# Kernel optimization log

Hardware: AMD Instinct MI355X
Metric: run time of the kernel (lower is better)

Reference implementation:

```python
import jax, jax.numpy as jnp
import numpy as np

EMBED = 1024
HEADS = 16
HEAD_DIM = EMBED // HEADS


def setup_inputs() -> dict:
    key = jax.random.key(0)
    ks = jax.random.split(key, 6)
    N, S = 4, 1024
    query = jax.random.normal(ks[0], (N, S, EMBED), dtype=jnp.float32)
    keys = jax.random.normal(ks[1], (N, S, EMBED), dtype=jnp.float32)
    values = jax.random.normal(ks[2], (N, S, EMBED), dtype=jnp.float32)
    mask = jax.random.randint(ks[3], (N, 1, S, S), 0, 2, dtype=jnp.int32)
    W_out = jax.random.normal(ks[4], (EMBED, EMBED), dtype=jnp.float32) * (1.0 / np.sqrt(EMBED))
    b_out = jax.random.normal(ks[5], (EMBED,), dtype=jnp.float32) * 0.02
    return {"query": query, "keys": keys, "values": values, "mask": mask,
            "W_out": W_out, "b_out": b_out}


def reference(query, keys, values, mask, W_out, b_out):
    N, Q, _ = query.shape
    K = keys.shape[1]
    # NOTE: the torch module never applies its per-head q/k/v Linear layers;
    # only the reshape + attention + fc_out are in the forward path.
    q = query.reshape(N, Q, HEADS, HEAD_DIM)
    k = keys.reshape(N, K, HEADS, HEAD_DIM)
    v = values.reshape(N, K, HEADS, HEAD_DIM)
    # energy: [N, H, Q, K]
    energy = jnp.einsum("bqhd,bkhd->bhqk", q, k)
    energy = jnp.where(mask == 0, jnp.float32(-1e20), energy)
    attn = jax.nn.softmax(energy / jnp.sqrt(jnp.float32(HEAD_DIM)), axis=3)
    out = jnp.einsum("bhqk,bkhd->bqhd", attn, v).reshape(N, Q, HEADS * HEAD_DIM)
    return out @ W_out.T + b_out
```

## Files before the change

kernel.cpp:

```cpp
#include <hip/hip_runtime.h>
#include <math.h>

#define NB 4
#define SL 1024
#define EMB 1024
#define NH 16
#define HD 64
#define QB 128

typedef __attribute__((ext_vector_type(8))) short bf16x8;
typedef __attribute__((ext_vector_type(4))) float f32x4;

static __device__ __forceinline__ unsigned pk2(float a, float b) {
    unsigned x = __float_as_uint(a) + 0x8000u;
    unsigned y = __float_as_uint(b) + 0x8000u;
    return (x >> 16) | (y & 0xFFFF0000u);
}
static __device__ __forceinline__ float exp2_fast(float x) {
    float r; asm("v_exp_f32 %0, %1" : "=v"(r) : "v"(x)); return r;
}
static __device__ __forceinline__ void gload_lds16(const void* g, void* l) {
    __builtin_amdgcn_global_load_lds(
        (const __attribute__((address_space(1))) unsigned int*)g,
        (__attribute__((address_space(3))) unsigned int*)l, 16, 0, 0);
}

__global__ __launch_bounds__(256) void prep(
    const float* __restrict__ W, unsigned short* __restrict__ Wb,
    const float* __restrict__ Kf, unsigned short* __restrict__ Kb,
    const float* __restrict__ V, unsigned short* __restrict__ Vt,
    const int* __restrict__ mask, unsigned long long* __restrict__ Mbt)
{
    __shared__ unsigned short sT[128 * 68];
    const int bid = blockIdx.x, tid = threadIdx.x;

    if (bid < 512) {
        int i = (bid * 256 + tid) * 8;
        float4 f0 = *(const float4*)&W[i];
        float4 f1 = *(const float4*)&W[i + 4];
        uint4 u = { pk2(f0.x,f0.y), pk2(f0.z,f0.w), pk2(f1.x,f1.y), pk2(f1.z,f1.w) };
        *(uint4*)&Wb[i] = u;
    } else if (bid < 2560) {
        int t = bid - 512;
        int b = t >> 9, h = (t >> 5) & 15, k0 = (t & 31) * 32;
        int r = tid >> 3, d = (tid & 7) * 8;
        const float* gp = &Kf[((size_t)(b * SL + k0 + r)) * EMB + h * HD + d];
        float4 f0 = *(const float4*)gp, f1 = *(const float4*)(gp + 4);
        uint4 u = { pk2(f0.x,f0.y), pk2(f0.z,f0.w), pk2(f1.x,f1.y), pk2(f1.z,f1.w) };
        *(uint4*)&Kb[((size_t)((b * NH + h) * SL + k0 + r)) * HD + d] = u;
    } else if (bid < 3072) {
        int t = bid - 2560;
        int bh = t >> 3, kb = t & 7;
        int b = bh >> 4, h = bh & 15;
        int k0 = kb * 128;
        #pragma unroll
        for (int i = 0; i < 4; ++i) {
            int lin = (i * 256 + tid) * 8;
            int r = lin >> 6, d = lin & 63;
            const float* gp = &V[((size_t)(b * SL + k0 + r)) * EMB + h * HD + d];
            float4 f0 = *(const float4*)gp, f1 = *(const float4*)(gp + 4);
            uint2 u0 = { pk2(f0.x,f0.y), pk2(f0.z,f0.w) };
            uint2 u1 = { pk2(f1.x,f1.y), pk2(f1.z,f1.w) };
            *(uint2*)&sT[r * 68 + d]     = u0;
            *(uint2*)&sT[r * 68 + d + 4] = u1;
        }
        __syncthreads();
        #pragma unroll
        for (int p = 0; p < 4; ++p) {
            int d = p * 16 + (tid >> 4);
            int c = tid & 15;
            unsigned v[4];
            #pragma unroll
            for (int j = 0; j < 4; ++j) {
                unsigned lo = sT[(c * 8 + 2 * j) * 68 + d];
                unsigned hi = sT[(c * 8 + 2 * j + 1) * 68 + d];
                v[j] = lo | (hi << 16);
            }
            uint4 u = { v[0], v[1], v[2], v[3] };
            *(uint4*)&Vt[((size_t)(bh * HD + d)) * SL + k0 + c * 8] = u;
        }
    } else {
        int t = bid - 3072;
        int lane = tid & 63;
        #pragma unroll
        for (int r = 0; r < 4; ++r) {
            int wid = (t * 4 + (tid >> 6)) * 4 + r;
            int c = wid & 15, q = (wid >> 4) & 1023, bb = wid >> 14;
            int mv = mask[((size_t)bb * SL + q) * SL + c * 64 + lane];
            unsigned long long bits = __ballot(mv != 0);
            if (lane == 0) Mbt[((size_t)bb * 16 + c) * SL + q] = bits;
        }
    }
}

__global__ __launch_bounds__(256, 2) void attn_mfma(
    const float* __restrict__ Q, const unsigned short* __restrict__ Kb,
    const unsigned short* __restrict__ Vt,
    const unsigned long long* __restrict__ Mbt,
    unsigned short* __restrict__ Oa)
{
    const int q0 = blockIdx.x * QB;
    const int h = blockIdx.y, b = blockIdx.z;
    const int tid = threadIdx.x;
    const int w = tid >> 6, lane = tid & 63;
    const int m16 = lane & 15, quad = lane >> 4;
    const int lr = lane >> 3, lc = lane & 7;
    const int sr0 = tid >> 3;

    __shared__ __align__(16) unsigned short sQ[QB * 64];
    __shared__ __align__(16) unsigned short sK[2][64 * 64];
    __shared__ __align__(16) unsigned short sVt[2][64 * 64];
    __shared__ __align__(16) unsigned short sP[QB * 72];
    __shared__ uint2 lut[16];

    if (tid < 16) {
        unsigned w0 = ((tid & 1) ? 0xFFFFu : 0u) | ((tid & 2) ? 0xFFFF0000u : 0u);
        unsigned w1 = ((tid & 4) ? 0xFFFFu : 0u) | ((tid & 8) ? 0xFFFF0000u : 0u);
        lut[tid] = make_uint2(w0, w1);
    }

    const size_t vbase = (size_t)((b * NH + h) * HD) * SL;
    const size_t kbase = (size_t)((b * NH + h) * SL) * HD;

    #pragma unroll
    for (int i = 0; i < 2; ++i) {
        int row = w * 16 + i * 8;
        gload_lds16(&Vt[vbase + (size_t)(row + lr) * SL + (lc ^ lr) * 8], &sVt[0][row * 64]);
        gload_lds16(&Kb[kbase + (size_t)(row + lr) * HD + (lc ^ lr) * 8], &sK[0][row * 64]);
    }
    #pragma unroll
    for (int it = 0; it < 4; ++it) {
        int r = sr0 + it * 32;
        const float* gp = &Q[((size_t)(b * SL + q0 + r)) * EMB + h * HD + lc * 8];
        float4 f0 = *(const float4*)gp, f1 = *(const float4*)(gp + 4);
        uint4 u = { pk2(f0.x,f0.y), pk2(f0.z,f0.w), pk2(f1.x,f1.y), pk2(f1.z,f1.w) };
        *(uint4*)&sQ[r * 64 + ((lc ^ (r & 7)) * 8)] = u;
    }
    __syncthreads();

    bf16x8 bQ[2][2];
    #pragma unroll
    for (int u = 0; u < 2; ++u) {
        int qrow = w * 32 + u * 16 + m16;
        #pragma unroll
        for (int hh = 0; hh < 2; ++hh)
            bQ[u][hh] = *(const bf16x8*)&sQ[qrow * 64 + (((hh * 4 + quad) ^ (qrow & 7)) * 8)];
    }

    f32x4 O[2][4] = {};
    f32x4 lacc[2] = {};
    const float CSC = 0.125f * 1.44269504f;
    const short one_bf = (short)0x3F80;
    const bf16x8 ones = { one_bf, one_bf, one_bf, one_bf, one_bf, one_bf, one_bf, one_bf };

    for (int kt = 0; kt < 16; ++kt) {
        const int bf = kt & 1;
        if (kt < 15) {
            const int k0n = (kt + 1) * 64;
            #pragma unroll
            for (int i = 0; i < 2; ++i) {
                int row = w * 16 + i * 8;
                gload_lds16(&Vt[vbase + (size_t)(row + lr) * SL + k0n + (lc ^ lr) * 8],
                            &sVt[bf ^ 1][row * 64]);
                gload_lds16(&Kb[kbase + (size_t)(k0n + row + lr) * HD + (lc ^ lr) * 8],
                            &sK[bf ^ 1][row * 64]);
            }
        }
        unsigned long long mb0 = Mbt[(size_t)(b * 16 + kt) * SL + q0 + w * 32 + m16];
        unsigned long long mb1 = Mbt[(size_t)(b * 16 + kt) * SL + q0 + w * 32 + 16 + m16];

        f32x4 sc[2][4];
        #pragma unroll
        for (int t = 0; t < 4; ++t) {
            int krow = t * 16 + m16;
            bf16x8 a0 = *(const bf16x8*)&sK[bf][krow * 64 + ((quad ^ (krow & 7)) * 8)];
            bf16x8 a1 = *(const bf16x8*)&sK[bf][krow * 64 + (((4 + quad) ^ (krow & 7)) * 8)];
            f32x4 z = {0.f, 0.f, 0.f, 0.f};
            sc[0][t] = __builtin_amdgcn_mfma_f32_16x16x32_bf16(a0, bQ[0][0], z,        0,0,0);
            sc[0][t] = __builtin_amdgcn_mfma_f32_16x16x32_bf16(a1, bQ[0][1], sc[0][t], 0,0,0);
            sc[1][t] = __builtin_amdgcn_mfma_f32_16x16x32_bf16(a0, bQ[1][0], z,        0,0,0);
            sc[1][t] = __builtin_amdgcn_mfma_f32_16x16x32_bf16(a1, bQ[1][1], sc[1][t], 0,0,0);
        }

        #pragma unroll
        for (int u = 0; u < 2; ++u) {
            unsigned long long mb = u ? mb1 : mb0;
            unsigned wlo = (unsigned)mb, whi = (unsigned)(mb >> 32);
            unsigned short* pr = &sP[(w * 32 + u * 16 + m16) * 72];
            #pragma unroll
            for (int t = 0; t < 4; ++t) {
                unsigned word = (t < 2) ? wlo : whi;
                unsigned nib = (word >> ((t & 1) * 16 + quad * 4)) & 0xFu;
                uint2 am = lut[nib];
                uint2 pw;
                pw.x = pk2(exp2_fast(sc[u][t][0] * CSC), exp2_fast(sc[u][t][1] * CSC)) & am.x;
                pw.y = pk2(exp2_fast(sc[u][t][2] * CSC), exp2_fast(sc[u][t][3] * CSC)) & am.y;
                *(uint2*)&pr[t * 16 + quad * 4] = pw;
            }
        }
        asm volatile("s_waitcnt lgkmcnt(0)" ::: "memory");

        bf16x8 bP[2][2];
        #pragma unroll
        for (int u = 0; u < 2; ++u)
            #pragma unroll
            for (int hh = 0; hh < 2; ++hh)
                bP[u][hh] = *(const bf16x8*)&sP[(w * 32 + u * 16 + m16) * 72 + hh * 32 + quad * 8];

        lacc[0] = __builtin_amdgcn_mfma_f32_16x16x32_bf16(ones, bP[0][0], lacc[0], 0,0,0);
        lacc[0] = __builtin_amdgcn_mfma_f32_16x16x32_bf16(ones, bP[0][1], lacc[0], 0,0,0);
        lacc[1] = __builtin_amdgcn_mfma_f32_16x16x32_bf16(ones, bP[1][0], lacc[1], 0,0,0);
        lacc[1] = __builtin_amdgcn_mfma_f32_16x16x32_bf16(ones, bP[1][1], lacc[1], 0,0,0);

        #pragma unroll
        for (int dt = 0; dt < 4; ++dt) {
            int drow = dt * 16 + m16;
            bf16x8 v0 = *(const bf16x8*)&sVt[bf][drow * 64 + ((quad ^ (drow & 7)) * 8)];
            bf16x8 v1 = *(const bf16x8*)&sVt[bf][drow * 64 + (((4 + quad) ^ (drow & 7)) * 8)];
            O[0][dt] = __builtin_amdgcn_mfma_f32_16x16x32_bf16(v0, bP[0][0], O[0][dt], 0,0,0);
            O[0][dt] = __builtin_amdgcn_mfma_f32_16x16x32_bf16(v1, bP[0][1], O[0][dt], 0,0,0);
            O[1][dt] = __builtin_amdgcn_mfma_f32_16x16x32_bf16(v0, bP[1][0], O[1][dt], 0,0,0);
            O[1][dt] = __builtin_amdgcn_mfma_f32_16x16x32_bf16(v1, bP[1][1], O[1][dt], 0,0,0);
        }

        __syncthreads();
    }

    #pragma unroll
    for (int u = 0; u < 2; ++u) {
        float inv = 1.f / lacc[u][0];
        size_t base = ((size_t)(b * SL + q0 + w * 32 + u * 16 + m16)) * EMB + h * HD + quad * 4;
        #pragma unroll
        for (int dt = 0; dt < 4; ++dt) {
            uint2 ow = { pk2(O[u][dt][0] * inv, O[u][dt][1] * inv),
                         pk2(O[u][dt][2] * inv, O[u][dt][3] * inv) };
            *(uint2*)&Oa[base + dt * 16] = ow;
        }
    }
}

__global__ __launch_bounds__(512, 2) void proj_mfma(
    const unsigned short* __restrict__ A, const unsigned short* __restrict__ Wb,
    const float* __restrict__ bias, float* __restrict__ C)
{
    const int n0 = blockIdx.x * 128;
    const int m0 = blockIdx.y * 128;
    const int tid = threadIdx.x;
    const int w = tid >> 6, lane = tid & 63;
    const int m16 = lane & 15, quad = lane >> 4;
    const int lr = lane >> 3, lc = lane & 7;
    const int wm = (w >> 2) * 64, wn = (w & 3) * 32;

    __shared__ __align__(16) unsigned short sA[2][128 * 64];
    __shared__ __align__(16) unsigned short sW[2][128 * 64];

    f32x4 acc[4][2] = {};

    #pragma unroll
    for (int i = 0; i < 2; ++i) {
        int r = w * 16 + i * 8;
        gload_lds16(&A [(size_t)(m0 + r + lr) * EMB + (lc ^ lr) * 8], &sA[0][r * 64]);
        gload_lds16(&Wb[(size_t)(n0 + r + lr) * EMB + (lc ^ lr) * 8], &sW[0][r * 64]);
    }
    __syncthreads();

    for (int it = 0; it < 16; ++it) {
        const int bf = it & 1;
        if (it < 15) {
            int e0 = (it + 1) * 64;
            #pragma unroll
            for (int i = 0; i < 2; ++i) {
                int r = w * 16 + i * 8;
                gload_lds16(&A [(size_t)(m0 + r + lr) * EMB + e0 + (lc ^ lr) * 8], &sA[bf ^ 1][r * 64]);
                gload_lds16(&Wb[(size_t)(n0 + r + lr) * EMB + e0 + (lc ^ lr) * 8], &sW[bf ^ 1][r * 64]);
            }
        }
        #pragma unroll
        for (int hh = 0; hh < 2; ++hh) {
            bf16x8 af[4], bw[2];
            #pragma unroll
            for (int mt = 0; mt < 4; ++mt) {
                int r = wm + mt * 16 + m16;
                af[mt] = *(const bf16x8*)&sA[bf][r * 64 + (((hh * 4 + quad) ^ (r & 7)) * 8)];
            }
            #pragma unroll
            for (int nt = 0; nt < 2; ++nt) {
                int r = wn + nt * 16 + m16;
                bw[nt] = *(const bf16x8*)&sW[bf][r * 64 + (((hh * 4 + quad) ^ (r & 7)) * 8)];
            }
            #pragma unroll
            for (int mt = 0; mt < 4; ++mt)
                #pragma unroll
                for (int nt = 0; nt < 2; ++nt)
                    acc[mt][nt] = __builtin_amdgcn_mfma_f32_16x16x32_bf16(af[mt], bw[nt], acc[mt][nt], 0,0,0);
        }
        __syncthreads();
    }

    #pragma unroll
    for (int nt = 0; nt < 2; ++nt) {
        float bv = bias[n0 + wn + nt * 16 + m16];
        #pragma unroll
        for (int mt = 0; mt < 4; ++mt) {
            size_t row = (size_t)(m0 + wm + mt * 16 + quad * 4);
            #pragma unroll
            for (int rg = 0; rg < 4; ++rg)
                C[(row + rg) * EMB + n0 + wn + nt * 16 + m16] = acc[mt][nt][rg] + bv;
        }
    }
}

extern "C" void kernel_launch(void* const* d_in, const int* in_sizes, int n_in,
                              void* d_out, int out_size, void* d_ws, size_t ws_size,
                              hipStream_t stream) {
    const float* Q    = (const float*)d_in[0];
    const float* K    = (const float*)d_in[1];
    const float* V    = (const float*)d_in[2];
    const int*   mask = (const int*)  d_in[3];
    const float* W    = (const float*)d_in[4];
    const float* bias = (const float*)d_in[5];

    unsigned short* Oa = (unsigned short*)d_ws;
    unsigned short* Wb = Oa + (size_t)NB * SL * EMB;
    unsigned long long* Mbt = (unsigned long long*)(Wb + (size_t)EMB * EMB);
    unsigned short* Vt = (unsigned short*)(Mbt + (size_t)NB * 16 * SL);
    unsigned short* Kb = Vt + (size_t)NB * NH * HD * SL;

    prep<<<7168, 256, 0, stream>>>(W, Wb, K, Kb, V, Vt, mask, Mbt);
    attn_mfma<<<dim3(SL / QB, NH, NB), 256, 0, stream>>>(Q, Kb, Vt, Mbt, Oa);
    proj_mfma<<<dim3(EMB / 128, (NB * SL) / 128), 512, 0, stream>>>(Oa, Wb, bias, (float*)d_out);
}
```

Baseline: 166.0 us.

## Pre-convert Q to bf16 in prep, share Q/P LDS buffer, remap attention blocks

Q is now converted to bf16 in a head-major layout inside the prep kernel, so the attention kernel loads it with direct global-to-LDS copies instead of fp32 loads plus in-kernel packing. The Q and P shared-memory buffers are merged into one, which needs an extra barrier after Q is read into registers. The mask LUT is replaced by bitwise computation, and the grid is flattened with a block remap that groups 8 heads per query tile, likely for L2 reuse. The trade is extra prep traffic for writing and re-reading Qb, against less LDS per block, which may allow higher occupancy.

Result: slower. 172.4 us (+3.9%).

```diff
diff --git a/kernel.cpp b/kernel.cpp
--- a/kernel.cpp
+++ b/kernel.cpp
@@ -28,6 +28,7 @@
 __global__ __launch_bounds__(256) void prep(
     const float* __restrict__ W, unsigned short* __restrict__ Wb,
     const float* __restrict__ Kf, unsigned short* __restrict__ Kb,
+    const float* __restrict__ Qf, unsigned short* __restrict__ Qb,
     const float* __restrict__ V, unsigned short* __restrict__ Vt,
     const int* __restrict__ mask, unsigned long long* __restrict__ Mbt)
 {
@@ -40,16 +41,19 @@
         float4 f1 = *(const float4*)&W[i + 4];
         uint4 u = { pk2(f0.x,f0.y), pk2(f0.z,f0.w), pk2(f1.x,f1.y), pk2(f1.z,f1.w) };
         *(uint4*)&Wb[i] = u;
-    } else if (bid < 2560) {
+    } else if (bid < 4608) {
         int t = bid - 512;
+        const float* src = Kf;
+        unsigned short* dst = Kb;
+        if (t >= 2048) { t -= 2048; src = Qf; dst = Qb; }
         int b = t >> 9, h = (t >> 5) & 15, k0 = (t & 31) * 32;
         int r = tid >> 3, d = (tid & 7) * 8;
-        const float* gp = &Kf[((size_t)(b * SL + k0 + r)) * EMB + h * HD + d];
+        const float* gp = &src[((size_t)(b * SL + k0 + r)) * EMB + h * HD + d];
         float4 f0 = *(const float4*)gp, f1 = *(const float4*)(gp + 4);
         uint4 u = { pk2(f0.x,f0.y), pk2(f0.z,f0.w), pk2(f1.x,f1.y), pk2(f1.z,f1.w) };
-        *(uint4*)&Kb[((size_t)((b * NH + h) * SL + k0 + r)) * HD + d] = u;
-    } else if (bid < 3072) {
-        int t = bid - 2560;
+        *(uint4*)&dst[((size_t)((b * NH + h) * SL + k0 + r)) * HD + d] = u;
+    } else if (bid < 5120) {
+        int t = bid - 4608;
         int bh = t >> 3, kb = t & 7;
         int b = bh >> 4, h = bh & 15;
         int k0 = kb * 128;
@@ -80,7 +84,7 @@
             *(uint4*)&Vt[((size_t)(bh * HD + d)) * SL + k0 + c * 8] = u;
         }
     } else {
-        int t = bid - 3072;
+        int t = bid - 5120;
         int lane = tid & 63;
         #pragma unroll
         for (int r = 0; r < 4; ++r) {
@@ -94,30 +98,24 @@
 }
 
 __global__ __launch_bounds__(256, 2) void attn_mfma(
-    const float* __restrict__ Q, const unsigned short* __restrict__ Kb,
+    const unsigned short* __restrict__ Qb, const unsigned short* __restrict__ Kb,
     const unsigned short* __restrict__ Vt,
     const unsigned long long* __restrict__ Mbt,
     unsigned short* __restrict__ Oa)
 {
-    const int q0 = blockIdx.x * QB;
-    const int h = blockIdx.y, b = blockIdx.z;
+    const int bid = blockIdx.x;
+    const int bh  = ((bid >> 6) << 3) | (bid & 7);
+    const int q0  = ((bid >> 3) & 7) * QB;
+    const int b = bh >> 4, h = bh & 15;
+
     const int tid = threadIdx.x;
     const int w = tid >> 6, lane = tid & 63;
     const int m16 = lane & 15, quad = lane >> 4;
     const int lr = lane >> 3, lc = lane & 7;
-    const int sr0 = tid >> 3;
-
-    __shared__ __align__(16) unsigned short sQ[QB * 64];
+
+    __shared__ __align__(16) unsigned short sQP[QB * 72];
     __shared__ __align__(16) unsigned short sK[2][64 * 64];
     __shared__ __align__(16) unsigned short sVt[2][64 * 64];
-    __shared__ __align__(16) unsigned short sP[QB * 72];
-    __shared__ uint2 lut[16];
-
-    if (tid < 16) {
-        unsigned w0 = ((tid & 1) ? 0xFFFFu : 0u) | ((tid & 2) ? 0xFFFF0000u : 0u);
-        unsigned w1 = ((tid & 4) ? 0xFFFFu : 0u) | ((tid & 8) ? 0xFFFF0000u : 0u);
-        lut[tid] = make_uint2(w0, w1);
-    }
 
     const size_t vbase = (size_t)((b * NH + h) * HD) * SL;
     const size_t kbase = (size_t)((b * NH + h) * SL) * HD;
@@ -129,12 +127,9 @@
         gload_lds16(&Kb[kbase + (size_t)(row + lr) * HD + (lc ^ lr) * 8], &sK[0][row * 64]);
     }
     #pragma unroll
-    for (int it = 0; it < 4; ++it) {
-        int r = sr0 + it * 32;
-        const float* gp = &Q[((size_t)(b * SL + q0 + r)) * EMB + h * HD + lc * 8];
-        float4 f0 = *(const float4*)gp, f1 = *(const float4*)(gp + 4);
-        uint4 u = { pk2(f0.x,f0.y), pk2(f0.z,f0.w), pk2(f1.x,f1.y), pk2(f1.z,f1.w) };
-        *(uint4*)&sQ[r * 64 + ((lc ^ (r & 7)) * 8)] = u;
+    for (int i = 0; i < 4; ++i) {
+        int row = w * 32 + i * 8;
+        gload_lds16(&Qb[kbase + (size_t)(q0 + row + lr) * HD + (lc ^ lr) * 8], &sQP[row * 64]);
     }
     __syncthreads();
 
@@ -144,8 +139,9 @@
         int qrow = w * 32 + u * 16 + m16;
         #pragma unroll
         for (int hh = 0; hh < 2; ++hh)
-            bQ[u][hh] = *(const bf16x8*)&sQ[qrow * 64 + (((hh * 4 + quad) ^ (qrow & 7)) * 8)];
-    }
+            bQ[u][hh] = *(const bf16x8*)&sQP[qrow * 64 + (((hh * 4 + quad) ^ (qrow & 7)) * 8)];
+    }
+    __syncthreads();
 
     f32x4 O[2][4] = {};
     f32x4 lacc[2] = {};
@@ -186,15 +182,16 @@
         for (int u = 0; u < 2; ++u) {
             unsigned long long mb = u ? mb1 : mb0;
             unsigned wlo = (unsigned)mb, whi = (unsigned)(mb >> 32);
-            unsigned short* pr = &sP[(w * 32 + u * 16 + m16) * 72];
+            unsigned short* pr = &sQP[(w * 32 + u * 16 + m16) * 72];
             #pragma unroll
             for (int t = 0; t < 4; ++t) {
                 unsigned word = (t < 2) ? wlo : whi;
                 unsigned nib = (word >> ((t & 1) * 16 + quad * 4)) & 0xFu;
-                uint2 am = lut[nib];
+                unsigned am0 = ((nib & 1u) ? 0xFFFFu : 0u) | ((nib & 2u) ? 0xFFFF0000u : 0u);
+                unsigned am1 = ((nib & 4u) ? 0xFFFFu : 0u) | ((nib & 8u) ? 0xFFFF0000u : 0u);
                 uint2 pw;
-                pw.x = pk2(exp2_fast(sc[u][t][0] * CSC), exp2_fast(sc[u][t][1] * CSC)) & am.x;
-                pw.y = pk2(exp2_fast(sc[u][t][2] * CSC), exp2_fast(sc[u][t][3] * CSC)) & am.y;
+                pw.x = pk2(exp2_fast(sc[u][t][0] * CSC), exp2_fast(sc[u][t][1] * CSC)) & am0;
+                pw.y = pk2(exp2_fast(sc[u][t][2] * CSC), exp2_fast(sc[u][t][3] * CSC)) & am1;
                 *(uint2*)&pr[t * 16 + quad * 4] = pw;
             }
         }
@@ -205,7 +202,7 @@
         for (int u = 0; u < 2; ++u)
             #pragma unroll
             for (int hh = 0; hh < 2; ++hh)
-                bP[u][hh] = *(const bf16x8*)&sP[(w * 32 + u * 16 + m16) * 72 + hh * 32 + quad * 8];
+                bP[u][hh] = *(const bf16x8*)&sQP[(w * 32 + u * 16 + m16) * 72 + hh * 32 + quad * 8];
 
         lacc[0] = __builtin_amdgcn_mfma_f32_16x16x32_bf16(ones, bP[0][0], lacc[0], 0,0,0);
         lacc[0] = __builtin_amdgcn_mfma_f32_16x16x32_bf16(ones, bP[0][1], lacc[0], 0,0,0);
@@ -325,8 +322,9 @@
     unsigned long long* Mbt = (unsigned long long*)(Wb + (size_t)EMB * EMB);
     unsigned short* Vt = (unsigned short*)(Mbt + (size_t)NB * 16 * SL);
     unsigned short* Kb = Vt + (size_t)NB * NH * HD * SL;
-
-    prep<<<7168, 256, 0, stream>>>(W, Wb, K, Kb, V, Vt, mask, Mbt);
-    attn_mfma<<<dim3(SL / QB, NH, NB), 256, 0, stream>>>(Q, Kb, Vt, Mbt, Oa);
+    unsigned short* Qbuf = Kb + (size_t)NB * NH * SL * HD;
+
+    prep<<<9216, 256, 0, stream>>>(W, Wb, K, Kb, Q, Qbuf, V, Vt, mask, Mbt);
+    attn_mfma<<<512, 256, 0, stream>>>(Qbuf, Kb, Vt, Mbt, Oa);
     proj_mfma<<<dim3(EMB / 128, (NB * SL) / 128), 512, 0, stream>>>(Oa, Wb, bias, (float*)d_out);
 }
```

## Halve attention query tile, reuse Q LDS for P, raise occupancy and swizzle grid

Applied to the files above, without the earlier changes.

Shrinks the attention query block from 128 to 64 rows so each wave handles 16 query rows, doubling the block count to 1024 and raising launch bounds to 4 blocks per CU. The sQ buffer is reused as the P staging buffer, and the mask LUT in LDS is replaced by inline bit computation, which cuts LDS footprint. A 1D grid with a remapped block index groups blocks so those sharing K/V run close together. This aims at better latency hiding and L2 reuse, at the cost of reloading K/V tiles for twice as many blocks and fewer MFMAs per K/V load.

New measurement: 167.5 us. Within noise of the previous version (+0.9%).

```diff
diff --git a/kernel.cpp b/kernel.cpp
--- a/kernel.cpp
+++ b/kernel.cpp
@@ -6,7 +6,7 @@
 #define EMB 1024
 #define NH 16
 #define HD 64
-#define QB 128
+#define QB 64
 
 typedef __attribute__((ext_vector_type(8))) short bf16x8;
 typedef __attribute__((ext_vector_type(4))) float f32x4;
@@ -93,31 +93,26 @@
     }
 }
 
-__global__ __launch_bounds__(256, 2) void attn_mfma(
-    const float* __restrict__ Q, const unsigned short* __restrict__ Kb,
+__global__ __launch_bounds__(256, 4) void attn_mfma(
+    const float* __restrict__ Qf, const unsigned short* __restrict__ Kb,
     const unsigned short* __restrict__ Vt,
     const unsigned long long* __restrict__ Mbt,
     unsigned short* __restrict__ Oa)
 {
-    const int q0 = blockIdx.x * QB;
-    const int h = blockIdx.y, b = blockIdx.z;
+    const int bid = blockIdx.x;
+    const int bh  = ((bid >> 7) << 3) | (bid & 7);
+    const int q0  = ((bid >> 3) & 15) * QB;
+    const int b = bh >> 4, h = bh & 15;
+
     const int tid = threadIdx.x;
     const int w = tid >> 6, lane = tid & 63;
     const int m16 = lane & 15, quad = lane >> 4;
     const int lr = lane >> 3, lc = lane & 7;
     const int sr0 = tid >> 3;
 
-    __shared__ __align__(16) unsigned short sQ[QB * 64];
-    __shared__ __align__(16) unsigned short sK[2][64 * 64];
+    __shared__ __align__(16) unsigned short sQP[QB * 64];
+    __shared__ __align__(16) unsigned short sK [2][64 * 64];
     __shared__ __align__(16) unsigned short sVt[2][64 * 64];
-    __shared__ __align__(16) unsigned short sP[QB * 72];
-    __shared__ uint2 lut[16];
-
-    if (tid < 16) {
-        unsigned w0 = ((tid & 1) ? 0xFFFFu : 0u) | ((tid & 2) ? 0xFFFF0000u : 0u);
-        unsigned w1 = ((tid & 4) ? 0xFFFFu : 0u) | ((tid & 8) ? 0xFFFF0000u : 0u);
-        lut[tid] = make_uint2(w0, w1);
-    }
 
     const size_t vbase = (size_t)((b * NH + h) * HD) * SL;
     const size_t kbase = (size_t)((b * NH + h) * SL) * HD;
@@ -129,26 +124,24 @@
         gload_lds16(&Kb[kbase + (size_t)(row + lr) * HD + (lc ^ lr) * 8], &sK[0][row * 64]);
     }
     #pragma unroll
-    for (int it = 0; it < 4; ++it) {
+    for (int it = 0; it < 2; ++it) {
         int r = sr0 + it * 32;
-        const float* gp = &Q[((size_t)(b * SL + q0 + r)) * EMB + h * HD + lc * 8];
+        const float* gp = &Qf[((size_t)(b * SL + q0 + r)) * EMB + h * HD + lc * 8];
         float4 f0 = *(const float4*)gp, f1 = *(const float4*)(gp + 4);
         uint4 u = { pk2(f0.x,f0.y), pk2(f0.z,f0.w), pk2(f1.x,f1.y), pk2(f1.z,f1.w) };
-        *(uint4*)&sQ[r * 64 + ((lc ^ (r & 7)) * 8)] = u;
+        *(uint4*)&sQP[r * 64 + ((lc ^ (r & 7)) * 8)] = u;
     }
     __syncthreads();
 
-    bf16x8 bQ[2][2];
-    #pragma unroll
-    for (int u = 0; u < 2; ++u) {
-        int qrow = w * 32 + u * 16 + m16;
-        #pragma unroll
-        for (int hh = 0; hh < 2; ++hh)
-            bQ[u][hh] = *(const bf16x8*)&sQ[qrow * 64 + (((hh * 4 + quad) ^ (qrow & 7)) * 8)];
-    }
-
-    f32x4 O[2][4] = {};
-    f32x4 lacc[2] = {};
+    const int qrow = w * 16 + m16;
+    bf16x8 bQ[2];
+    #pragma unroll
+    for (int hh = 0; hh < 2; ++hh)
+        bQ[hh] = *(const bf16x8*)&sQP[qrow * 64 + (((hh * 4 + quad) ^ (qrow & 7)) * 8)];
+    __syncthreads();
+
+    f32x4 O[4] = {};
+    f32x4 lacc = {};
     const float CSC = 0.125f * 1.44269504f;
     const short one_bf = (short)0x3F80;
     const bf16x8 ones = { one_bf, one_bf, one_bf, one_bf, one_bf, one_bf, one_bf, one_bf };
@@ -166,74 +159,63 @@
                             &sK[bf ^ 1][row * 64]);
             }
         }
-        unsigned long long mb0 = Mbt[(size_t)(b * 16 + kt) * SL + q0 + w * 32 + m16];
-        unsigned long long mb1 = Mbt[(size_t)(b * 16 + kt) * SL + q0 + w * 32 + 16 + m16];
-
-        f32x4 sc[2][4];
+        unsigned long long mb = Mbt[(size_t)(b * 16 + kt) * SL + q0 + qrow];
+
+        f32x4 sc[4];
         #pragma unroll
         for (int t = 0; t < 4; ++t) {
             int krow = t * 16 + m16;
             bf16x8 a0 = *(const bf16x8*)&sK[bf][krow * 64 + ((quad ^ (krow & 7)) * 8)];
             bf16x8 a1 = *(const bf16x8*)&sK[bf][krow * 64 + (((4 + quad) ^ (krow & 7)) * 8)];
             f32x4 z = {0.f, 0.f, 0.f, 0.f};
-            sc[0][t] = __builtin_amdgcn_mfma_f32_16x16x32_bf16(a0, bQ[0][0], z,        0,0,0);
-            sc[0][t] = __builtin_amdgcn_mfma_f32_16x16x32_bf16(a1, bQ[0][1], sc[0][t], 0,0,0);
-            sc[1][t] = __builtin_amdgcn_mfma_f32_16x16x32_bf16(a0, bQ[1][0], z,        0,0,0);
-            sc[1][t] = __builtin_amdgcn_mfma_f32_16x16x32_bf16(a1, bQ[1][1], sc[1][t], 0,0,0);
-        }
-
-        #pragma unroll
-        for (int u = 0; u < 2; ++u) {
-            unsigned long long mb = u ? mb1 : mb0;
+            sc[t] = __builtin_amdgcn_mfma_f32_16x16x32_bf16(a0, bQ[0], z,     0, 0, 0);
+            sc[t] = __builtin_amdgcn_mfma_f32_16x16x32_bf16(a1, bQ[1], sc[t], 0, 0, 0);
+        }
+
+        {
             unsigned wlo = (unsigned)mb, whi = (unsigned)(mb >> 32);
-            unsigned short* pr = &sP[(w * 32 + u * 16 + m16) * 72];
             #pragma unroll
             for (int t = 0; t < 4; ++t) {
                 unsigned word = (t < 2) ? wlo : whi;
                 unsigned nib = (word >> ((t & 1) * 16 + quad * 4)) & 0xFu;
-                uint2 am = lut[nib];
+                unsigned am0 = ((nib & 1u) ? 0xFFFFu : 0u) | ((nib & 2u) ? 0xFFFF0000u : 0u);
+                unsigned am1 = ((nib & 4u) ? 0xFFFFu : 0u) | ((nib & 8u) ? 0xFFFF0000u : 0u);
                 uint2 pw;
-                pw.x = pk2(exp2_fast(sc[u][t][0] * CSC), exp2_fast(sc[u][t][1] * CSC)) & am.x;
-                pw.y = pk2(exp2_fast(sc[u][t][2] * CSC), exp2_fast(sc[u][t][3] * CSC)) & am.y;
-                *(uint2*)&pr[t * 16 + quad * 4] = pw;
+                pw.x = pk2(exp2_fast(sc[t][0] * CSC), exp2_fast(sc[t][1] * CSC)) & am0;
+                pw.y = pk2(exp2_fast(sc[t][2] * CSC), exp2_fast(sc[t][3] * CSC)) & am1;
+                int c = 2 * t + (quad >> 1);
+                *(uint2*)&sQP[qrow * 64 + ((c ^ (qrow & 7)) * 8 + (quad & 1) * 4)] = pw;
             }
         }
         asm volatile("s_waitcnt lgkmcnt(0)" ::: "memory");
 
-        bf16x8 bP[2][2];
-        #pragma unroll
-        for (int u = 0; u < 2; ++u)
-            #pragma unroll
-            for (int hh = 0; hh < 2; ++hh)
-                bP[u][hh] = *(const bf16x8*)&sP[(w * 32 + u * 16 + m16) * 72 + hh * 32 + quad * 8];
-
-        lacc[0] = __builtin_amdgcn_mfma_f32_16x16x32_bf16(ones, bP[0][0], lacc[0], 0,0,0);
-        lacc[0] = __builtin_amdgcn_mfma_f32_16x16x32_bf16(ones, bP[0][1], lacc[0], 0,0,0);
-        lacc[1] = __builtin_amdgcn_mfma_f32_16x16x32_bf16(ones, bP[1][0], lacc[1], 0,0,0);
-        lacc[1] = __builtin_amdgcn_mfma_f32_16x16x32_bf16(ones, bP[1][1], lacc[1], 0,0,0);
+        bf16x8 bP[2];
+        #pragma unroll
+        for (int hh = 0; hh < 2; ++hh)
+            bP[hh] = *(const bf16x8*)&sQP[qrow * 64 + (((hh * 4 + quad) ^ (qrow & 7)) * 8)];
+
+        lacc = __builtin_amdgcn_mfma_f32_16x16x32_bf16(ones, bP[0], lacc, 0, 0, 0);
+        lacc = __builtin_amdgcn_mfma_f32_16x16x32_bf16(ones, bP[1], lacc, 0, 0, 0);
 
         #pragma unroll
         for (int dt = 0; dt < 4; ++dt) {
             int drow = dt * 16 + m16;
             bf16x8 v0 = *(const bf16x8*)&sVt[bf][drow * 64 + ((quad ^ (drow & 7)) * 8)];
             bf16x8 v1 = *(const bf16x8*)&sVt[bf][drow * 64 + (((4 + quad) ^ (drow & 7)) * 8)];
-            O[0][dt] = __builtin_amdgcn_mfma_f32_16x16x32_bf16(v0, bP[0][0], O[0][dt], 0,0,0);
-            O[0][dt] = __builtin_amdgcn_mfma_f32_16x16x32_bf16(v1, bP[0][1], O[0][dt], 0,0,0);
-            O[1][dt] = __builtin_amdgcn_mfma_f32_16x16x32_bf16(v0, bP[1][0], O[1][dt], 0,0,0);
-            O[1][dt] = __builtin_amdgcn_mfma_f32_16x16x32_bf16(v1, bP[1][1], O[1][dt], 0,0,0);
+            O[dt] = __builtin_amdgcn_mfma_f32_16x16x32_bf16(v0, bP[0], O[dt], 0, 0, 0);
+            O[dt] = __builtin_amdgcn_mfma_f32_16x16x32_bf16(v1, bP[1], O[dt], 0, 0, 0);
         }
 
         __syncthreads();
     }
 
-    #pragma unroll
-    for (int u = 0; u < 2; ++u) {
-        float inv = 1.f / lacc[u][0];
-        size_t base = ((size_t)(b * SL + q0 + w * 32 + u * 16 + m16)) * EMB + h * HD + quad * 4;
+    {
+        float inv = 1.f / lacc[0];
+        size_t base = ((size_t)(b * SL + q0 + qrow)) * EMB + h * HD + quad * 4;
         #pragma unroll
         for (int dt = 0; dt < 4; ++dt) {
-            uint2 ow = { pk2(O[u][dt][0] * inv, O[u][dt][1] * inv),
-                         pk2(O[u][dt][2] * inv, O[u][dt][3] * inv) };
+            uint2 ow = { pk2(O[dt][0] * inv, O[dt][1] * inv),
+                         pk2(O[dt][2] * inv, O[dt][3] * inv) };
             *(uint2*)&Oa[base + dt * 16] = ow;
         }
     }
@@ -327,6 +309,6 @@
     unsigned short* Kb = Vt + (size_t)NB * NH * HD * SL;
 
     prep<<<7168, 256, 0, stream>>>(W, Wb, K, Kb, V, Vt, mask, Mbt);
-    attn_mfma<<<dim3(SL / QB, NH, NB), 256, 0, stream>>>(Q, Kb, Vt, Mbt, Oa);
+    attn_mfma<<<1024, 256, 0, stream>>>(Q, Kb, Vt, Mbt, Oa);
     proj_mfma<<<dim3(EMB / 128, (NB * SL) / 128), 512, 0, stream>>>(Oa, Wb, bias, (float*)d_out);
 }
```
